# Kernel optimization log

Hardware: AMD Instinct MI355X
Metric: run time of the kernel (lower is better)

Reference implementation:

```python
import jax, jax.numpy as jnp
import numpy as np

GAMMA = 0.7
ALPHA = 1.0
EPS = 1e-6

def setup_inputs() -> dict:
    key = jax.random.key(0)
    k1, k2 = jax.random.split(key)
    x = jax.random.normal(k1, (1, 4096, 1024), dtype=jnp.float32)
    attn = jax.random.uniform(k2, (1, 4096, 4096), dtype=jnp.float32)
    return {"x": x, "attn": attn, "layer_idx": 10, "total_layers": 12}


def reference(x, attn, layer_idx, total_layers):
    B, N, D = x.shape  # module's masking/cat logic requires B == 1
    if layer_idx < GAMMA * total_layers:
        return x

    # --- spatial autocorrelation score s ---
    a = x.mean(axis=-1)                                            # [B,N]
    z = (a - a.mean(1, keepdims=True)) / (a.std(1, ddof=1, keepdims=True) + EPS)
    # diag(z z^T * W) == z^2 * diag(W): skip the O(N^2) outer product
    I_l = z * z * jnp.diagonal(attn, axis1=-2, axis2=-1)           # [B,N]
    s = (I_l - I_l.mean(1, keepdims=True)) / (I_l.std(1, ddof=1, keepdims=True) + EPS)

    # --- threshold (torch.median returns the LOWER middle for even N) ---
    mu_s = s.mean(1, keepdims=True)
    abs_med = jnp.sort(jnp.abs(s), axis=1)[:, (N - 1) // 2][:, None]
    lb = ALPHA * (mu_s - abs_med)
    ub = ALPHA * (mu_s + abs_med)
    mask_A = (s < lb) | (s > ub)                                   # [B,N]

    xb = x[0]
    mA = mask_A[0]
    idx = jnp.arange(N)
    n_A = mA.sum()

    # compact A tokens to the front preserving original order
    orderA = jnp.argsort(~mA, stable=True)
    tokA = xb[orderA]                    # first n_A rows are tokens_A, rest are B tokens (masked later)
    mid = n_A // 2
    n2 = n_A - mid                       # number of A2 tokens

    # A1[i] = tokA[i] (valid i < mid); A2[j] = tokA[mid + j] (valid j < n2)
    A2 = jnp.take(tokA, jnp.clip(mid + idx, 0, N - 1), axis=0)     # [N,D] padded
    validA1 = idx < mid
    validA2 = idx < n2

    sim = tokA @ A2.T                                              # [N,N]
    sim = jnp.where(validA2[None, :], sim, -jnp.inf)
    matches = jnp.argmax(sim, axis=1)                              # [N]
    merged = 0.5 * (tokA + A2[matches])
    merged = jnp.where(validA1[:, None], merged, 0.0)              # rows >= mid zeroed

    # residual A2 tokens (not matched by any valid A1 row), compacted and zero-padded
    drop_idx = jnp.where(validA1, matches, N)                      # OOB index dropped
    matched = jnp.zeros(N, bool).at[drop_idx].set(True, mode='drop')
    resid_valid = validA2 & ~matched
    orderR = jnp.argsort(~resid_valid, stable=True)
    residual = jnp.where(resid_valid[orderR][:, None], A2[orderR], 0.0)  # [N,D]

    # B tokens compacted, then merged tokens appended, zero pad to N
    n_B = N - n_A
    orderB = jnp.argsort(mA, stable=True)
    tokB = jnp.where((idx < n_B)[:, None], xb[orderB], 0.0)        # [N,D]
    shift = jnp.clip(idx - n_B, 0, N - 1)
    in_merged = ((idx >= n_B) & (idx < n_B + mid)).astype(xb.dtype)[:, None]
    out = (tokB + in_merged * merged[shift])[None]                 # [1,N,D]
    return out, residual
```

## Files before the change

### kernel.cpp

```cpp
#include <hip/hip_runtime.h>

#define N 4096
#define D 1024
#define EPSF 1e-6f

typedef _Float16 f16;
typedef f16 f16x8 __attribute__((ext_vector_type(8)));
typedef float f32x4 __attribute__((ext_vector_type(4)));
typedef unsigned long long u64;

#define PLANE ((size_t)2048 * 1024)

struct WS {
  int n_A, mid, n2, n_B, n_resid, pad[3];
  float a[N];
  float diag[N];
  int A1idx[N];
  int A2idx[N];
  int Bidx[N];
  int matches[N];
  int residIdx[N];
  u64 bestKey[2048];
};

__device__ __forceinline__ u64 packKey(float v, int j) {
  unsigned u = __float_as_uint(v);
  unsigned m = (u & 0x80000000u) ? ~u : (u | 0x80000000u);
  return ((u64)m << 32) | (unsigned)(~(unsigned)j);
}

__global__ __launch_bounds__(256) void k_prep(const float* __restrict__ x,
                                              const float* __restrict__ attn, WS* ws) {
  int row = blockIdx.x;
  int t = threadIdx.x;
  float4 v = ((const float4*)(x + (size_t)row * D))[t];
  float sm = v.x + v.y + v.z + v.w;
  for (int o = 32; o; o >>= 1) sm += __shfl_down(sm, o, 64);
  __shared__ float w[4];
  if ((t & 63) == 0) w[t >> 6] = sm;
  __syncthreads();
  if (t == 0) {
    ws->a[row] = (w[0] + w[1] + w[2] + w[3]) * (1.0f / D);
    ws->diag[row] = attn[(size_t)row * N + row];
  }
}

__global__ __launch_bounds__(256) void k_mask(WS* ws) {
  __shared__ double dred[4], dred2[4];
  __shared__ float bcast[2];
  __shared__ int hist[256];
  __shared__ int wsum[4];
  __shared__ unsigned sPrefix;
  __shared__ int sRank;
  int tid = threadIdx.x;
  int lane = tid & 63, wv = tid >> 6;

  #pragma unroll
  for (int q = 0; q < 8; q++) ws->bestKey[tid * 8 + q] = 0ull;

  float av[16];
  double s = 0.0, s2 = 0.0;
  #pragma unroll
  for (int q = 0; q < 4; q++) {
    float4 va = ((const float4*)ws->a)[tid * 4 + q];
    float f4[4] = {va.x, va.y, va.z, va.w};
    #pragma unroll
    for (int e = 0; e < 4; e++) {
      av[q * 4 + e] = f4[e];
      s += f4[e]; s2 += (double)f4[e] * f4[e];
    }
  }
  for (int o = 32; o; o >>= 1) { s += __shfl_down(s, o, 64); s2 += __shfl_down(s2, o, 64); }
  if (lane == 0) { dred[wv] = s; dred2[wv] = s2; }
  __syncthreads();
  if (tid == 0) {
    double t1 = dred[0] + dred[1] + dred[2] + dred[3];
    double t2 = dred2[0] + dred2[1] + dred2[2] + dred2[3];
    bcast[0] = (float)(t1 / N);
    bcast[1] = (float)sqrt((t2 - t1 * t1 / N) / (N - 1));
  }
  __syncthreads();
  float meanA = bcast[0], stdA = bcast[1];

  float il[16];
  s = 0.0; s2 = 0.0;
  #pragma unroll
  for (int q = 0; q < 4; q++) {
    float4 dg = ((const float4*)ws->diag)[tid * 4 + q];
    float d4[4] = {dg.x, dg.y, dg.z, dg.w};
    #pragma unroll
    for (int e = 0; e < 4; e++) {
      float z = (av[q * 4 + e] - meanA) / (stdA + EPSF);
      float I = z * z * d4[e];
      il[q * 4 + e] = I;
      s += I; s2 += (double)I * I;
    }
  }
  for (int o = 32; o; o >>= 1) { s += __shfl_down(s, o, 64); s2 += __shfl_down(s2, o, 64); }
  __syncthreads();
  if (lane == 0) { dred[wv] = s; dred2[wv] = s2; }
  __syncthreads();
  if (tid == 0) {
    double t1 = dred[0] + dred[1] + dred[2] + dred[3];
    double t2 = dred2[0] + dred2[1] + dred2[2] + dred2[3];
    bcast[0] = (float)(t1 / N);
    bcast[1] = (float)sqrt((t2 - t1 * t1 / N) / (N - 1));
    sPrefix = 0u; sRank = (N - 1) / 2;
  }
  __syncthreads();
  float meanI = bcast[0], stdI = bcast[1];

  float sv[16]; unsigned ab[16];
  #pragma unroll
  for (int q = 0; q < 16; q++) {
    float sval = (il[q] - meanI) / (stdI + EPSF);
    sv[q] = sval;
    ab[q] = __float_as_uint(fabsf(sval));
  }

  for (int p = 3; p >= 0; p--) {
    hist[tid] = 0;
    __syncthreads();
    unsigned pre = sPrefix;
    int rk = sRank;
    int sh = p * 8;
    unsigned mHi = (p == 3) ? 0u : (0xFFFFFFFFu << (sh + 8));
    #pragma unroll
    for (int q = 0; q < 16; q++)
      if ((ab[q] & mHi) == pre) atomicAdd(&hist[(ab[q] >> sh) & 255], 1);
    __syncthreads();
    int v2 = hist[tid];
    int inc = v2;
    #pragma unroll
    for (int o = 1; o < 64; o <<= 1) { int u = __shfl_up(inc, o, 64); if (lane >= o) inc += u; }
    if (lane == 63) wsum[wv] = inc;
    __syncthreads();
    if (tid == 0) { wsum[1] += wsum[0]; wsum[2] += wsum[1]; wsum[3] += wsum[2]; }
    __syncthreads();
    int incl = (wv ? wsum[wv - 1] : 0) + inc;
    int E = incl - v2;
    if (v2 && rk >= E && rk < E + v2) {
      sPrefix = pre | ((unsigned)tid << sh);
      sRank = rk - E;
    }
    __syncthreads();
  }
  float med = __uint_as_float(sPrefix);

  int msk[16], loc[16]; int tot = 0;
  #pragma unroll
  for (int q = 0; q < 16; q++) {
    bool m = fabsf(sv[q]) > med;
    msk[q] = m; loc[q] = tot; tot += (int)m;
  }
  int inc = tot;
  #pragma unroll
  for (int o = 1; o < 64; o <<= 1) { int u = __shfl_up(inc, o, 64); if (lane >= o) inc += u; }
  if (lane == 63) wsum[wv] = inc;
  __syncthreads();
  if (tid == 0) { wsum[1] += wsum[0]; wsum[2] += wsum[1]; wsum[3] += wsum[2]; }
  __syncthreads();
  int nA = wsum[3];
  int base = (wv ? wsum[wv - 1] : 0) + inc - tot;
  int midl = nA >> 1;
  #pragma unroll
  for (int q = 0; q < 16; q++) {
    int i = tid * 16 + q;
    int r = base + loc[q];
    if (msk[q]) {
      if (r < midl) ws->A1idx[r] = i; else ws->A2idx[r - midl] = i;
    } else {
      ws->Bidx[i - r] = i;
    }
  }
  if (tid == 0) { ws->n_A = nA; ws->mid = midl; ws->n2 = nA - midl; ws->n_B = N - nA; }
}

__global__ __launch_bounds__(128) void k_pack(const float* __restrict__ x,
                                              f16* __restrict__ PAhi, f16* __restrict__ PAlo,
                                              f16* __restrict__ PBhi, f16* __restrict__ PBlo,
                                              WS* ws) {
  int b = blockIdx.x, t = threadIdx.x;
  const float* src;
  f16 *dh, *dl;
  int j;
  if (b < 2048) {
    if (b >= ws->mid) return;
    j = b;
    src = x + (size_t)ws->A1idx[b] * D;
    dh = PAhi; dl = PAlo;
  } else {
    j = b - 2048;
    if (j >= ws->n2) return;
    src = x + (size_t)ws->A2idx[j] * D;
    dh = PBhi; dl = PBlo;
  }
  float4 v0 = ((const float4*)src)[t * 2];
  float4 v1 = ((const float4*)src)[t * 2 + 1];
  float vv[8] = {v0.x, v0.y, v0.z, v0.w, v1.x, v1.y, v1.z, v1.w};
  f16x8 h, l;
  #pragma unroll
  for (int q = 0; q < 8; q++) {
    f16 hq = (f16)vv[q];
    h[q] = hq;
    l[q] = (f16)(vv[q] - (float)hq);
  }
  int rt = j >> 6, rl = j & 63;
  int kt = t >> 3, gl = t & 7;
  size_t off = ((size_t)(rt * 16 + kt) << 12) + rl * 64 + ((gl ^ (rl & 7)) * 8);
  *(f16x8*)(dh + off) = h;
  *(f16x8*)(dl + off) = l;
}

__global__ __launch_bounds__(256) void k_gemm(const f16* __restrict__ PAhi,
                                              const f16* __restrict__ PAlo,
                                              const f16* __restrict__ PBhi,
                                              const f16* __restrict__ PBlo, WS* ws) {
  const int mid = ws->mid, n2 = ws->n2;
  int L = blockIdx.x;
  int local = L >> 3;
  int bj = ((L & 7) << 1) | (local >> 4);
  int bi = local & 15;
  if (bi * 64 >= mid || bj * 64 >= n2) return;

  __shared__ f16 lds[2][4][64 * 64];

  const int tid = threadIdx.x;
  const int lane = tid & 63;
  const int wid = tid >> 6;
  const int wr = wid >> 1, wc = wid & 1;

  const f16* plane = (wid == 0) ? PAhi : (wid == 1) ? PAlo : (wid == 2) ? PBhi : PBlo;
  const int ptile = (wid < 2) ? bi : bj;

  f16x8 pr[8];
  auto LOAD = [&](int t) {
    const f16* tb = plane + ((size_t)((ptile << 4) + t) << 12);
    #pragma unroll
    for (int i = 0; i < 8; i++) pr[i] = *(const f16x8*)(tb + i * 512 + lane * 8);
  };
  auto STORE = [&](int buf) {
    #pragma unroll
    for (int i = 0; i < 8; i++) *(f16x8*)&lds[buf][wid][i * 512 + lane * 8] = pr[i];
  };

  const int colg = lane & 15, rowg = lane >> 4;
  const int ma0 = wr * 32 + colg, ma1 = ma0 + 16;
  const int mb0 = wc * 32 + colg, mb1 = mb0 + 16;

  f32x4 zero = {0.f, 0.f, 0.f, 0.f};
  f32x4 acc[2][2];
  acc[0][0] = zero; acc[0][1] = zero; acc[1][0] = zero; acc[1][1] = zero;

#define FRAG(buf, t4, row, g) \
  (*(const f16x8*)&lds[buf][t4][(row) * 64 + ((((g) ^ ((row) & 7))) * 8)])

  LOAD(0);
  STORE(0);
  __syncthreads();
  for (int t16 = 0; t16 < 16; t16++) {
    int buf = t16 & 1;
    if (t16 < 15) LOAD(t16 + 1);
    #pragma unroll
    for (int ks = 0; ks < 2; ks++) {
      int gk = ks * 4 + rowg;
      f16x8 ah0 = FRAG(buf, 0, ma0, gk), ah1 = FRAG(buf, 0, ma1, gk);
      f16x8 al0 = FRAG(buf, 1, ma0, gk), al1 = FRAG(buf, 1, ma1, gk);
      f16x8 bh0 = FRAG(buf, 2, mb0, gk), bh1 = FRAG(buf, 2, mb1, gk);
      f16x8 bl0 = FRAG(buf, 3, mb0, gk), bl1 = FRAG(buf, 3, mb1, gk);
      acc[0][0] = __builtin_amdgcn_mfma_f32_16x16x32_f16(ah0, bh0, acc[0][0], 0, 0, 0);
      acc[0][0] = __builtin_amdgcn_mfma_f32_16x16x32_f16(ah0, bl0, acc[0][0], 0, 0, 0);
      acc[0][0] = __builtin_amdgcn_mfma_f32_16x16x32_f16(al0, bh0, acc[0][0], 0, 0, 0);
      acc[0][1] = __builtin_amdgcn_mfma_f32_16x16x32_f16(ah0, bh1, acc[0][1], 0, 0, 0);
      acc[0][1] = __builtin_amdgcn_mfma_f32_16x16x32_f16(ah0, bl1, acc[0][1], 0, 0, 0);
      acc[0][1] = __builtin_amdgcn_mfma_f32_16x16x32_f16(al0, bh1, acc[0][1], 0, 0, 0);
      acc[1][0] = __builtin_amdgcn_mfma_f32_16x16x32_f16(ah1, bh0, acc[1][0], 0, 0, 0);
      acc[1][0] = __builtin_amdgcn_mfma_f32_16x16x32_f16(ah1, bl0, acc[1][0], 0, 0, 0);
      acc[1][0] = __builtin_amdgcn_mfma_f32_16x16x32_f16(al1, bh0, acc[1][0], 0, 0, 0);
      acc[1][1] = __builtin_amdgcn_mfma_f32_16x16x32_f16(ah1, bh1, acc[1][1], 0, 0, 0);
      acc[1][1] = __builtin_amdgcn_mfma_f32_16x16x32_f16(ah1, bl1, acc[1][1], 0, 0, 0);
      acc[1][1] = __builtin_amdgcn_mfma_f32_16x16x32_f16(al1, bh1, acc[1][1], 0, 0, 0);
    }
    if (t16 < 15) {
      __syncthreads();
      STORE(buf ^ 1);
      __syncthreads();
    }
  }
#undef FRAG

  #pragma unroll
  for (int mi = 0; mi < 2; mi++) {
    #pragma unroll
    for (int i = 0; i < 4; i++) {
      int grow = bi * 64 + wr * 32 + mi * 16 + rowg * 4 + i;
      u64 key = 0;
      #pragma unroll
      for (int ni = 0; ni < 2; ni++) {
        int gcol = bj * 64 + wc * 32 + ni * 16 + colg;
        if (gcol < n2) {
          u64 k2 = packKey(acc[mi][ni][i], gcol);
          if (k2 > key) key = k2;
        }
      }
      #pragma unroll
      for (int m = 8; m; m >>= 1) {
        u64 o = (u64)__shfl_xor((long long)key, m, 64);
        if (o > key) key = o;
      }
      if (colg == 0 && grow < mid && key) atomicMax(&ws->bestKey[grow], key);
    }
  }
}

__global__ __launch_bounds__(1024) void k_match(WS* ws) {
  __shared__ int flag[N];
  __shared__ int wsum[16];
  int tid = threadIdx.x;
  int lane = tid & 63, wv = tid >> 6;
  int mid = ws->mid, n2 = ws->n2;
  #pragma unroll
  for (int q = 0; q < 4; q++) flag[tid * 4 + q] = 0;
  __syncthreads();
  #pragma unroll
  for (int q = 0; q < 2; q++) {
    int r = tid + q * 1024;
    if (r < mid) {
      int j = (int)(~(unsigned)(ws->bestKey[r] & 0xffffffffull));
      ws->matches[r] = j;
      flag[j] = 1;
    }
  }
  __syncthreads();
  int v[4], loc[4]; int tot = 0;
  #pragma unroll
  for (int q = 0; q < 4; q++) {
    int j = tid * 4 + q;
    bool val = (j < n2) && (flag[j] == 0);
    v[q] = val; loc[q] = tot; tot += (int)val;
  }
  int inc = tot;
  #pragma unroll
  for (int o = 1; o < 64; o <<= 1) { int u = __shfl_up(inc, o, 64); if (lane >= o) inc += u; }
  if (lane == 63) wsum[wv] = inc;
  __syncthreads();
  if (tid < 16) {
    int t = wsum[tid];
    #pragma unroll
    for (int o = 1; o < 16; o <<= 1) { int u = __shfl_up(t, o, 64); if (tid >= o) t += u; }
    wsum[tid] = t;
  }
  __syncthreads();
  int base = (wv ? wsum[wv - 1] : 0) + inc - tot;
  #pragma unroll
  for (int q = 0; q < 4; q++)
    if (v[q]) ws->residIdx[base + loc[q]] = ws->A2idx[tid * 4 + q];
  if (tid == 0) ws->n_resid = wsum[15];
}

__global__ __launch_bounds__(256) void k_write(const float* __restrict__ x,
                                               float* __restrict__ out, WS* ws) {
  int r = blockIdx.x;
  int t = threadIdx.x;
  int n_B = ws->n_B, mid = ws->mid, n_resid = ws->n_resid;
  float4 res = make_float4(0.f, 0.f, 0.f, 0.f);
  if (r < N) {
    if (r < n_B) {
      res = ((const float4*)(x + (size_t)ws->Bidx[r] * D))[t];
    } else if (r < n_B + mid) {
      int m = r - n_B;
      float4 v1 = ((const float4*)(x + (size_t)ws->A1idx[m] * D))[t];
      float4 v2 = ((const float4*)(x + (size_t)ws->A2idx[ws->matches[m]] * D))[t];
      res = make_float4(0.5f * (v1.x + v2.x), 0.5f * (v1.y + v2.y),
                        0.5f * (v1.z + v2.z), 0.5f * (v1.w + v2.w));
    }
  } else {
    int k = r - N;
    if (k < n_resid) {
      res = ((const float4*)(x + (size_t)ws->residIdx[k] * D))[t];
    }
  }
  ((float4*)(out + (size_t)r * D))[t] = res;
}

extern "C" void kernel_launch(void* const* d_in, const int* in_sizes, int n_in,
                              void* d_out, int out_size, void* d_ws, size_t ws_size,
                              hipStream_t stream) {
  const float* x = (const float*)d_in[0];
  const float* attn = (const float*)d_in[1];
  float* out = (float*)d_out;
  WS* ws = (WS*)d_ws;
  f16* PAhi = (f16*)d_out;
  f16* PAlo = PAhi + PLANE;
  f16* PBhi = PAlo + PLANE;
  f16* PBlo = PBhi + PLANE;

  k_prep<<<N, 256, 0, stream>>>(x, attn, ws);
  k_mask<<<1, 256, 0, stream>>>(ws);
  k_pack<<<4096, 128, 0, stream>>>(x, PAhi, PAlo, PBhi, PBlo, ws);
  k_gemm<<<256, 256, 0, stream>>>(PAhi, PAlo, PBhi, PBlo, ws);
  k_match<<<1, 1024, 0, stream>>>(ws);
  k_write<<<2 * N, 256, 0, stream>>>(x, out, ws);
}
```

Before: 58.18 us.

## Fuse all stages into one cooperative persistent kernel with grid syncs

Replaces the six separate launches (prep, mask, pack, gemm, match, write) with a single cooperative kernel of 256 blocks. Stages are separated by grid.sync, and each stage's work is redistributed over the fixed block count with strided loops. The intent is to remove per-launch overhead and the inter-kernel gaps around the two single-block serial stages. In exchange it adds grid-wide barrier costs, and the memory-bound write and pack phases now run at low occupancy (one block per CU looping), which may reduce achieved bandwidth.

```diff
diff --git a/kernel.cpp b/kernel.cpp
--- a/kernel.cpp
+++ b/kernel.cpp
@@ -1,4 +1,7 @@
 #include <hip/hip_runtime.h>
+#include <hip/hip_cooperative_groups.h>
+
+namespace cg = cooperative_groups;
 
 #define N 4096
 #define D 1024
@@ -23,364 +26,377 @@
   u64 bestKey[2048];
 };
 
+struct MaskSh {
+  double dred[4], dred2[4];
+  float bcast[2];
+  int hist[256];
+  int wsum[4];
+  unsigned sPrefix;
+  int sRank;
+};
+
 __device__ __forceinline__ u64 packKey(float v, int j) {
   unsigned u = __float_as_uint(v);
   unsigned m = (u & 0x80000000u) ? ~u : (u | 0x80000000u);
   return ((u64)m << 32) | (unsigned)(~(unsigned)j);
 }
 
-__global__ __launch_bounds__(256) void k_prep(const float* __restrict__ x,
-                                              const float* __restrict__ attn, WS* ws) {
-  int row = blockIdx.x;
-  int t = threadIdx.x;
-  float4 v = ((const float4*)(x + (size_t)row * D))[t];
-  float sm = v.x + v.y + v.z + v.w;
-  for (int o = 32; o; o >>= 1) sm += __shfl_down(sm, o, 64);
-  __shared__ float w[4];
-  if ((t & 63) == 0) w[t >> 6] = sm;
-  __syncthreads();
-  if (t == 0) {
-    ws->a[row] = (w[0] + w[1] + w[2] + w[3]) * (1.0f / D);
-    ws->diag[row] = attn[(size_t)row * N + row];
-  }
-}
-
-__global__ __launch_bounds__(256) void k_mask(WS* ws) {
-  __shared__ double dred[4], dred2[4];
-  __shared__ float bcast[2];
-  __shared__ int hist[256];
-  __shared__ int wsum[4];
-  __shared__ unsigned sPrefix;
-  __shared__ int sRank;
-  int tid = threadIdx.x;
-  int lane = tid & 63, wv = tid >> 6;
-
-  #pragma unroll
-  for (int q = 0; q < 8; q++) ws->bestKey[tid * 8 + q] = 0ull;
-
-  float av[16];
-  double s = 0.0, s2 = 0.0;
-  #pragma unroll
-  for (int q = 0; q < 4; q++) {
-    float4 va = ((const float4*)ws->a)[tid * 4 + q];
-    float f4[4] = {va.x, va.y, va.z, va.w};
-    #pragma unroll
-    for (int e = 0; e < 4; e++) {
-      av[q * 4 + e] = f4[e];
-      s += f4[e]; s2 += (double)f4[e] * f4[e];
-    }
-  }
-  for (int o = 32; o; o >>= 1) { s += __shfl_down(s, o, 64); s2 += __shfl_down(s2, o, 64); }
-  if (lane == 0) { dred[wv] = s; dred2[wv] = s2; }
-  __syncthreads();
-  if (tid == 0) {
-    double t1 = dred[0] + dred[1] + dred[2] + dred[3];
-    double t2 = dred2[0] + dred2[1] + dred2[2] + dred2[3];
-    bcast[0] = (float)(t1 / N);
-    bcast[1] = (float)sqrt((t2 - t1 * t1 / N) / (N - 1));
-  }
-  __syncthreads();
-  float meanA = bcast[0], stdA = bcast[1];
-
-  float il[16];
-  s = 0.0; s2 = 0.0;
-  #pragma unroll
-  for (int q = 0; q < 4; q++) {
-    float4 dg = ((const float4*)ws->diag)[tid * 4 + q];
-    float d4[4] = {dg.x, dg.y, dg.z, dg.w};
-    #pragma unroll
-    for (int e = 0; e < 4; e++) {
-      float z = (av[q * 4 + e] - meanA) / (stdA + EPSF);
-      float I = z * z * d4[e];
-      il[q * 4 + e] = I;
-      s += I; s2 += (double)I * I;
-    }
-  }
-  for (int o = 32; o; o >>= 1) { s += __shfl_down(s, o, 64); s2 += __shfl_down(s2, o, 64); }
-  __syncthreads();
-  if (lane == 0) { dred[wv] = s; dred2[wv] = s2; }
-  __syncthreads();
-  if (tid == 0) {
-    double t1 = dred[0] + dred[1] + dred[2] + dred[3];
-    double t2 = dred2[0] + dred2[1] + dred2[2] + dred2[3];
-    bcast[0] = (float)(t1 / N);
-    bcast[1] = (float)sqrt((t2 - t1 * t1 / N) / (N - 1));
-    sPrefix = 0u; sRank = (N - 1) / 2;
-  }
-  __syncthreads();
-  float meanI = bcast[0], stdI = bcast[1];
-
-  float sv[16]; unsigned ab[16];
-  #pragma unroll
-  for (int q = 0; q < 16; q++) {
-    float sval = (il[q] - meanI) / (stdI + EPSF);
-    sv[q] = sval;
-    ab[q] = __float_as_uint(fabsf(sval));
-  }
-
-  for (int p = 3; p >= 0; p--) {
-    hist[tid] = 0;
-    __syncthreads();
-    unsigned pre = sPrefix;
-    int rk = sRank;
-    int sh = p * 8;
-    unsigned mHi = (p == 3) ? 0u : (0xFFFFFFFFu << (sh + 8));
-    #pragma unroll
-    for (int q = 0; q < 16; q++)
-      if ((ab[q] & mHi) == pre) atomicAdd(&hist[(ab[q] >> sh) & 255], 1);
-    __syncthreads();
-    int v2 = hist[tid];
-    int inc = v2;
-    #pragma unroll
-    for (int o = 1; o < 64; o <<= 1) { int u = __shfl_up(inc, o, 64); if (lane >= o) inc += u; }
-    if (lane == 63) wsum[wv] = inc;
-    __syncthreads();
-    if (tid == 0) { wsum[1] += wsum[0]; wsum[2] += wsum[1]; wsum[3] += wsum[2]; }
-    __syncthreads();
-    int incl = (wv ? wsum[wv - 1] : 0) + inc;
-    int E = incl - v2;
-    if (v2 && rk >= E && rk < E + v2) {
-      sPrefix = pre | ((unsigned)tid << sh);
-      sRank = rk - E;
-    }
-    __syncthreads();
-  }
-  float med = __uint_as_float(sPrefix);
-
-  int msk[16], loc[16]; int tot = 0;
-  #pragma unroll
-  for (int q = 0; q < 16; q++) {
-    bool m = fabsf(sv[q]) > med;
-    msk[q] = m; loc[q] = tot; tot += (int)m;
-  }
-  int inc = tot;
-  #pragma unroll
-  for (int o = 1; o < 64; o <<= 1) { int u = __shfl_up(inc, o, 64); if (lane >= o) inc += u; }
-  if (lane == 63) wsum[wv] = inc;
-  __syncthreads();
-  if (tid == 0) { wsum[1] += wsum[0]; wsum[2] += wsum[1]; wsum[3] += wsum[2]; }
-  __syncthreads();
-  int nA = wsum[3];
-  int base = (wv ? wsum[wv - 1] : 0) + inc - tot;
-  int midl = nA >> 1;
-  #pragma unroll
-  for (int q = 0; q < 16; q++) {
-    int i = tid * 16 + q;
-    int r = base + loc[q];
-    if (msk[q]) {
-      if (r < midl) ws->A1idx[r] = i; else ws->A2idx[r - midl] = i;
-    } else {
-      ws->Bidx[i - r] = i;
-    }
-  }
-  if (tid == 0) { ws->n_A = nA; ws->mid = midl; ws->n2 = nA - midl; ws->n_B = N - nA; }
-}
-
-__global__ __launch_bounds__(128) void k_pack(const float* __restrict__ x,
-                                              f16* __restrict__ PAhi, f16* __restrict__ PAlo,
-                                              f16* __restrict__ PBhi, f16* __restrict__ PBlo,
-                                              WS* ws) {
-  int b = blockIdx.x, t = threadIdx.x;
-  const float* src;
-  f16 *dh, *dl;
-  int j;
-  if (b < 2048) {
-    if (b >= ws->mid) return;
-    j = b;
-    src = x + (size_t)ws->A1idx[b] * D;
-    dh = PAhi; dl = PAlo;
-  } else {
-    j = b - 2048;
-    if (j >= ws->n2) return;
-    src = x + (size_t)ws->A2idx[j] * D;
-    dh = PBhi; dl = PBlo;
-  }
-  float4 v0 = ((const float4*)src)[t * 2];
-  float4 v1 = ((const float4*)src)[t * 2 + 1];
-  float vv[8] = {v0.x, v0.y, v0.z, v0.w, v1.x, v1.y, v1.z, v1.w};
-  f16x8 h, l;
-  #pragma unroll
-  for (int q = 0; q < 8; q++) {
-    f16 hq = (f16)vv[q];
-    h[q] = hq;
-    l[q] = (f16)(vv[q] - (float)hq);
-  }
-  int rt = j >> 6, rl = j & 63;
-  int kt = t >> 3, gl = t & 7;
-  size_t off = ((size_t)(rt * 16 + kt) << 12) + rl * 64 + ((gl ^ (rl & 7)) * 8);
-  *(f16x8*)(dh + off) = h;
-  *(f16x8*)(dl + off) = l;
-}
-
-__global__ __launch_bounds__(256) void k_gemm(const f16* __restrict__ PAhi,
-                                              const f16* __restrict__ PAlo,
-                                              const f16* __restrict__ PBhi,
-                                              const f16* __restrict__ PBlo, WS* ws) {
-  const int mid = ws->mid, n2 = ws->n2;
-  int L = blockIdx.x;
-  int local = L >> 3;
-  int bj = ((L & 7) << 1) | (local >> 4);
-  int bi = local & 15;
-  if (bi * 64 >= mid || bj * 64 >= n2) return;
-
-  __shared__ f16 lds[2][4][64 * 64];
+__global__ void __launch_bounds__(256) k_all(const float* __restrict__ x,
+                                             const float* __restrict__ attn,
+                                             f16* __restrict__ PAhi, f16* __restrict__ PAlo,
+                                             f16* __restrict__ PBhi, f16* __restrict__ PBlo,
+                                             float* __restrict__ out, WS* __restrict__ ws) {
+  cg::grid_group grid = cg::this_grid();
+  __shared__ __align__(16) f16 lds[2][4][64 * 64];
 
   const int tid = threadIdx.x;
   const int lane = tid & 63;
-  const int wid = tid >> 6;
-  const int wr = wid >> 1, wc = wid & 1;
-
-  const f16* plane = (wid == 0) ? PAhi : (wid == 1) ? PAlo : (wid == 2) ? PBhi : PBlo;
-  const int ptile = (wid < 2) ? bi : bj;
-
-  f16x8 pr[8];
-  auto LOAD = [&](int t) {
-    const f16* tb = plane + ((size_t)((ptile << 4) + t) << 12);
-    #pragma unroll
-    for (int i = 0; i < 8; i++) pr[i] = *(const f16x8*)(tb + i * 512 + lane * 8);
-  };
-  auto STORE = [&](int buf) {
-    #pragma unroll
-    for (int i = 0; i < 8; i++) *(f16x8*)&lds[buf][wid][i * 512 + lane * 8] = pr[i];
-  };
-
-  const int colg = lane & 15, rowg = lane >> 4;
-  const int ma0 = wr * 32 + colg, ma1 = ma0 + 16;
-  const int mb0 = wc * 32 + colg, mb1 = mb0 + 16;
-
-  f32x4 zero = {0.f, 0.f, 0.f, 0.f};
-  f32x4 acc[2][2];
-  acc[0][0] = zero; acc[0][1] = zero; acc[1][0] = zero; acc[1][1] = zero;
+  const int wv = tid >> 6;
+  const int bid = blockIdx.x;
+
+  {
+    #pragma unroll
+    for (int rr = 0; rr < 4; rr++) {
+      int row = bid * 16 + wv * 4 + rr;
+      const float4* xr = (const float4*)(x + (size_t)row * D);
+      float sm = 0.f;
+      #pragma unroll
+      for (int it = 0; it < 4; it++) {
+        float4 v = xr[it * 64 + lane];
+        sm += v.x + v.y + v.z + v.w;
+      }
+      for (int o = 32; o; o >>= 1) sm += __shfl_down(sm, o, 64);
+      if (lane == 0) {
+        ws->a[row] = sm * (1.0f / D);
+        ws->diag[row] = attn[(size_t)row * (N + 1)];
+      }
+    }
+  }
+  grid.sync();
+
+  if (bid == 0) {
+    MaskSh& sh = *(MaskSh*)lds;
+
+    #pragma unroll
+    for (int q = 0; q < 8; q++) ws->bestKey[tid * 8 + q] = 0ull;
+
+    float av[16];
+    double s = 0.0, s2 = 0.0;
+    #pragma unroll
+    for (int q = 0; q < 4; q++) {
+      float4 va = ((const float4*)ws->a)[tid * 4 + q];
+      float f4[4] = {va.x, va.y, va.z, va.w};
+      #pragma unroll
+      for (int e = 0; e < 4; e++) {
+        av[q * 4 + e] = f4[e];
+        s += f4[e]; s2 += (double)f4[e] * f4[e];
+      }
+    }
+    for (int o = 32; o; o >>= 1) { s += __shfl_down(s, o, 64); s2 += __shfl_down(s2, o, 64); }
+    if (lane == 0) { sh.dred[wv] = s; sh.dred2[wv] = s2; }
+    __syncthreads();
+    if (tid == 0) {
+      double t1 = sh.dred[0] + sh.dred[1] + sh.dred[2] + sh.dred[3];
+      double t2 = sh.dred2[0] + sh.dred2[1] + sh.dred2[2] + sh.dred2[3];
+      sh.bcast[0] = (float)(t1 / N);
+      sh.bcast[1] = (float)sqrt((t2 - t1 * t1 / N) / (N - 1));
+    }
+    __syncthreads();
+    float meanA = sh.bcast[0], stdA = sh.bcast[1];
+
+    float il[16];
+    s = 0.0; s2 = 0.0;
+    #pragma unroll
+    for (int q = 0; q < 4; q++) {
+      float4 dg = ((const float4*)ws->diag)[tid * 4 + q];
+      float d4[4] = {dg.x, dg.y, dg.z, dg.w};
+      #pragma unroll
+      for (int e = 0; e < 4; e++) {
+        float z = (av[q * 4 + e] - meanA) / (stdA + EPSF);
+        float I = z * z * d4[e];
+        il[q * 4 + e] = I;
+        s += I; s2 += (double)I * I;
+      }
+    }
+    for (int o = 32; o; o >>= 1) { s += __shfl_down(s, o, 64); s2 += __shfl_down(s2, o, 64); }
+    __syncthreads();
+    if (lane == 0) { sh.dred[wv] = s; sh.dred2[wv] = s2; }
+    __syncthreads();
+    if (tid == 0) {
+      double t1 = sh.dred[0] + sh.dred[1] + sh.dred[2] + sh.dred[3];
+      double t2 = sh.dred2[0] + sh.dred2[1] + sh.dred2[2] + sh.dred2[3];
+      sh.bcast[0] = (float)(t1 / N);
+      sh.bcast[1] = (float)sqrt((t2 - t1 * t1 / N) / (N - 1));
+      sh.sPrefix = 0u; sh.sRank = (N - 1) / 2;
+    }
+    __syncthreads();
+    float meanI = sh.bcast[0], stdI = sh.bcast[1];
+
+    float sv[16]; unsigned ab[16];
+    #pragma unroll
+    for (int q = 0; q < 16; q++) {
+      float sval = (il[q] - meanI) / (stdI + EPSF);
+      sv[q] = sval;
+      ab[q] = __float_as_uint(fabsf(sval));
+    }
+
+    for (int p = 3; p >= 0; p--) {
+      sh.hist[tid] = 0;
+      __syncthreads();
+      unsigned pre = sh.sPrefix;
+      int rk = sh.sRank;
+      int shf = p * 8;
+      unsigned mHi = (p == 3) ? 0u : (0xFFFFFFFFu << (shf + 8));
+      #pragma unroll
+      for (int q = 0; q < 16; q++)
+        if ((ab[q] & mHi) == pre) atomicAdd(&sh.hist[(ab[q] >> shf) & 255], 1);
+      __syncthreads();
+      int v2 = sh.hist[tid];
+      int inc = v2;
+      #pragma unroll
+      for (int o = 1; o < 64; o <<= 1) { int u = __shfl_up(inc, o, 64); if (lane >= o) inc += u; }
+      if (lane == 63) sh.wsum[wv] = inc;
+      __syncthreads();
+      if (tid == 0) { sh.wsum[1] += sh.wsum[0]; sh.wsum[2] += sh.wsum[1]; sh.wsum[3] += sh.wsum[2]; }
+      __syncthreads();
+      int incl = (wv ? sh.wsum[wv - 1] : 0) + inc;
+      int E = incl - v2;
+      if (v2 && rk >= E && rk < E + v2) {
+        sh.sPrefix = pre | ((unsigned)tid << shf);
+        sh.sRank = rk - E;
+      }
+      __syncthreads();
+    }
+    float med = __uint_as_float(sh.sPrefix);
+
+    int msk[16], loc[16]; int tot = 0;
+    #pragma unroll
+    for (int q = 0; q < 16; q++) {
+      bool m = fabsf(sv[q]) > med;
+      msk[q] = m; loc[q] = tot; tot += (int)m;
+    }
+    int inc = tot;
+    #pragma unroll
+    for (int o = 1; o < 64; o <<= 1) { int u = __shfl_up(inc, o, 64); if (lane >= o) inc += u; }
+    if (lane == 63) sh.wsum[wv] = inc;
+    __syncthreads();
+    if (tid == 0) { sh.wsum[1] += sh.wsum[0]; sh.wsum[2] += sh.wsum[1]; sh.wsum[3] += sh.wsum[2]; }
+    __syncthreads();
+    int nA = sh.wsum[3];
+    int base = (wv ? sh.wsum[wv - 1] : 0) + inc - tot;
+    int midl = nA >> 1;
+    #pragma unroll
+    for (int q = 0; q < 16; q++) {
+      int i = tid * 16 + q;
+      int r = base + loc[q];
+      if (msk[q]) {
+        if (r < midl) ws->A1idx[r] = i; else ws->A2idx[r - midl] = i;
+      } else {
+        ws->Bidx[i - r] = i;
+      }
+    }
+    if (tid == 0) { ws->n_A = nA; ws->mid = midl; ws->n2 = nA - midl; ws->n_B = N - nA; }
+  }
+  grid.sync();
+
+  const int mid = ws->mid, n2 = ws->n2;
+
+  {
+    int sub = tid >> 7;
+    int tt = tid & 127;
+    #pragma unroll 1
+    for (int it = 0; it < 8; it++) {
+      int slot = it * 512 + bid * 2 + sub;
+      const float* src = nullptr;
+      f16 *dh, *dl;
+      int j;
+      bool valid;
+      if (slot < 2048) {
+        j = slot; valid = (j < mid);
+        if (valid) src = x + (size_t)ws->A1idx[j] * D;
+        dh = PAhi; dl = PAlo;
+      } else {
+        j = slot - 2048; valid = (j < n2);
+        if (valid) src = x + (size_t)ws->A2idx[j] * D;
+        dh = PBhi; dl = PBlo;
+      }
+      if (valid) {
+        float4 v0 = ((const float4*)src)[tt * 2];
+        float4 v1 = ((const float4*)src)[tt * 2 + 1];
+        float vv[8] = {v0.x, v0.y, v0.z, v0.w, v1.x, v1.y, v1.z, v1.w};
+        f16x8 h, l;
+        #pragma unroll
+        for (int q = 0; q < 8; q++) {
+          f16 hq = (f16)vv[q];
+          h[q] = hq;
+          l[q] = (f16)(vv[q] - (float)hq);
+        }
+        int rt = j >> 6, rl = j & 63;
+        int kt = tt >> 3, gl = tt & 7;
+        size_t off = ((size_t)(rt * 16 + kt) << 12) + rl * 64 + ((gl ^ (rl & 7)) * 8);
+        *(f16x8*)(dh + off) = h;
+        *(f16x8*)(dl + off) = l;
+      }
+    }
+  }
+  grid.sync();
+
+  {
+    int local = bid >> 3;
+    int bj = ((bid & 7) << 1) | (local >> 4);
+    int bi = local & 15;
+    if (bi * 64 < mid && bj * 64 < n2) {
+      const int wid = wv;
+      const int wr = wid >> 1, wc = wid & 1;
+      const f16* plane = (wid == 0) ? PAhi : (wid == 1) ? PAlo : (wid == 2) ? PBhi : PBlo;
+      const int ptile = (wid < 2) ? bi : bj;
+
+      f16x8 pr[8];
+      auto LOAD = [&](int t) {
+        const f16* tb = plane + ((size_t)((ptile << 4) + t) << 12);
+        #pragma unroll
+        for (int i = 0; i < 8; i++) pr[i] = *(const f16x8*)(tb + i * 512 + lane * 8);
+      };
+      auto STORE = [&](int buf) {
+        #pragma unroll
+        for (int i = 0; i < 8; i++) *(f16x8*)&lds[buf][wid][i * 512 + lane * 8] = pr[i];
+      };
+
+      const int colg = lane & 15, rowg = lane >> 4;
+      const int ma0 = wr * 32 + colg, ma1 = ma0 + 16;
+      const int mb0 = wc * 32 + colg, mb1 = mb0 + 16;
+
+      f32x4 zero = {0.f, 0.f, 0.f, 0.f};
+      f32x4 acc[2][2];
+      acc[0][0] = zero; acc[0][1] = zero; acc[1][0] = zero; acc[1][1] = zero;
 
 #define FRAG(buf, t4, row, g) \
   (*(const f16x8*)&lds[buf][t4][(row) * 64 + ((((g) ^ ((row) & 7))) * 8)])
 
-  LOAD(0);
-  STORE(0);
-  __syncthreads();
-  for (int t16 = 0; t16 < 16; t16++) {
-    int buf = t16 & 1;
-    if (t16 < 15) LOAD(t16 + 1);
-    #pragma unroll
-    for (int ks = 0; ks < 2; ks++) {
-      int gk = ks * 4 + rowg;
-      f16x8 ah0 = FRAG(buf, 0, ma0, gk), ah1 = FRAG(buf, 0, ma1, gk);
-      f16x8 al0 = FRAG(buf, 1, ma0, gk), al1 = FRAG(buf, 1, ma1, gk);
-      f16x8 bh0 = FRAG(buf, 2, mb0, gk), bh1 = FRAG(buf, 2, mb1, gk);
-      f16x8 bl0 = FRAG(buf, 3, mb0, gk), bl1 = FRAG(buf, 3, mb1, gk);
-      acc[0][0] = __builtin_amdgcn_mfma_f32_16x16x32_f16(ah0, bh0, acc[0][0], 0, 0, 0);
-      acc[0][0] = __builtin_amdgcn_mfma_f32_16x16x32_f16(ah0, bl0, acc[0][0], 0, 0, 0);
-      acc[0][0] = __builtin_amdgcn_mfma_f32_16x16x32_f16(al0, bh0, acc[0][0], 0, 0, 0);
-      acc[0][1] = __builtin_amdgcn_mfma_f32_16x16x32_f16(ah0, bh1, acc[0][1], 0, 0, 0);
-      acc[0][1] = __builtin_amdgcn_mfma_f32_16x16x32_f16(ah0, bl1, acc[0][1], 0, 0, 0);
-      acc[0][1] = __builtin_amdgcn_mfma_f32_16x16x32_f16(al0, bh1, acc[0][1], 0, 0, 0);
-      acc[1][0] = __builtin_amdgcn_mfma_f32_16x16x32_f16(ah1, bh0, acc[1][0], 0, 0, 0);
-      acc[1][0] = __builtin_amdgcn_mfma_f32_16x16x32_f16(ah1, bl0, acc[1][0], 0, 0, 0);
-      acc[1][0] = __builtin_amdgcn_mfma_f32_16x16x32_f16(al1, bh0, acc[1][0], 0, 0, 0);
-      acc[1][1] = __builtin_amdgcn_mfma_f32_16x16x32_f16(ah1, bh1, acc[1][1], 0, 0, 0);
-      acc[1][1] = __builtin_amdgcn_mfma_f32_16x16x32_f16(ah1, bl1, acc[1][1], 0, 0, 0);
-      acc[1][1] = __builtin_amdgcn_mfma_f32_16x16x32_f16(al1, bh1, acc[1][1], 0, 0, 0);
-    }
-    if (t16 < 15) {
-      __syncthreads();
-      STORE(buf ^ 1);
-      __syncthreads();
-    }
-  }
+      LOAD(0);
+      STORE(0);
+      __syncthreads();
+      #pragma unroll 1
+      for (int t16 = 0; t16 < 16; t16++) {
+        int buf = t16 & 1;
+        if (t16 < 15) LOAD(t16 + 1);
+        #pragma unroll
+        for (int ks = 0; ks < 2; ks++) {
+          int gk = ks * 4 + rowg;
+          f16x8 ah0 = FRAG(buf, 0, ma0, gk), ah1 = FRAG(buf, 0, ma1, gk);
+          f16x8 al0 = FRAG(buf, 1, ma0, gk), al1 = FRAG(buf, 1, ma1, gk);
+          f16x8 bh0 = FRAG(buf, 2, mb0, gk), bh1 = FRAG(buf, 2, mb1, gk);
+          f16x8 bl0 = FRAG(buf, 3, mb0, gk), bl1 = FRAG(buf, 3, mb1, gk);
+          acc[0][0] = __builtin_amdgcn_mfma_f32_16x16x32_f16(ah0, bh0, acc[0][0], 0, 0, 0);
+          acc[0][0] = __builtin_amdgcn_mfma_f32_16x16x32_f16(ah0, bl0, acc[0][0], 0, 0, 0);
+          acc[0][0] = __builtin_amdgcn_mfma_f32_16x16x32_f16(al0, bh0, acc[0][0], 0, 0, 0);
+          acc[0][1] = __builtin_amdgcn_mfma_f32_16x16x32_f16(ah0, bh1, acc[0][1], 0, 0, 0);
+          acc[0][1] = __builtin_amdgcn_mfma_f32_16x16x32_f16(ah0, bl1, acc[0][1], 0, 0, 0);
+          acc[0][1] = __builtin_amdgcn_mfma_f32_16x16x32_f16(al0, bh1, acc[0][1], 0, 0, 0);
+          acc[1][0] = __builtin_amdgcn_mfma_f32_16x16x32_f16(ah1, bh0, acc[1][0], 0, 0, 0);
+          acc[1][0] = __builtin_amdgcn_mfma_f32_16x16x32_f16(ah1, bl0, acc[1][0], 0, 0, 0);
+          acc[1][0] = __builtin_amdgcn_mfma_f32_16x16x32_f16(al1, bh0, acc[1][0], 0, 0, 0);
+          acc[1][1] = __builtin_amdgcn_mfma_f32_16x16x32_f16(ah1, bh1, acc[1][1], 0, 0, 0);
+          acc[1][1] = __builtin_amdgcn_mfma_f32_16x16x32_f16(ah1, bl1, acc[1][1], 0, 0, 0);
+          acc[1][1] = __builtin_amdgcn_mfma_f32_16x16x32_f16(al1, bh1, acc[1][1], 0, 0, 0);
+        }
+        if (t16 < 15) {
+          __syncthreads();
+          STORE(buf ^ 1);
+          __syncthreads();
+        }
+      }
 #undef FRAG
 
-  #pragma unroll
-  for (int mi = 0; mi < 2; mi++) {
-    #pragma unroll
-    for (int i = 0; i < 4; i++) {
-      int grow = bi * 64 + wr * 32 + mi * 16 + rowg * 4 + i;
-      u64 key = 0;
-      #pragma unroll
-      for (int ni = 0; ni < 2; ni++) {
-        int gcol = bj * 64 + wc * 32 + ni * 16 + colg;
-        if (gcol < n2) {
-          u64 k2 = packKey(acc[mi][ni][i], gcol);
-          if (k2 > key) key = k2;
-        }
-      }
-      #pragma unroll
-      for (int m = 8; m; m >>= 1) {
-        u64 o = (u64)__shfl_xor((long long)key, m, 64);
-        if (o > key) key = o;
-      }
-      if (colg == 0 && grow < mid && key) atomicMax(&ws->bestKey[grow], key);
-    }
-  }
-}
-
-__global__ __launch_bounds__(1024) void k_match(WS* ws) {
-  __shared__ int flag[N];
-  __shared__ int wsum[16];
-  int tid = threadIdx.x;
-  int lane = tid & 63, wv = tid >> 6;
-  int mid = ws->mid, n2 = ws->n2;
-  #pragma unroll
-  for (int q = 0; q < 4; q++) flag[tid * 4 + q] = 0;
-  __syncthreads();
-  #pragma unroll
-  for (int q = 0; q < 2; q++) {
-    int r = tid + q * 1024;
-    if (r < mid) {
-      int j = (int)(~(unsigned)(ws->bestKey[r] & 0xffffffffull));
-      ws->matches[r] = j;
-      flag[j] = 1;
-    }
-  }
-  __syncthreads();
-  int v[4], loc[4]; int tot = 0;
-  #pragma unroll
-  for (int q = 0; q < 4; q++) {
-    int j = tid * 4 + q;
-    bool val = (j < n2) && (flag[j] == 0);
-    v[q] = val; loc[q] = tot; tot += (int)val;
-  }
-  int inc = tot;
-  #pragma unroll
-  for (int o = 1; o < 64; o <<= 1) { int u = __shfl_up(inc, o, 64); if (lane >= o) inc += u; }
-  if (lane == 63) wsum[wv] = inc;
-  __syncthreads();
-  if (tid < 16) {
-    int t = wsum[tid];
-    #pragma unroll
-    for (int o = 1; o < 16; o <<= 1) { int u = __shfl_up(t, o, 64); if (tid >= o) t += u; }
-    wsum[tid] = t;
-  }
-  __syncthreads();
-  int base = (wv ? wsum[wv - 1] : 0) + inc - tot;
-  #pragma unroll
-  for (int q = 0; q < 4; q++)
-    if (v[q]) ws->residIdx[base + loc[q]] = ws->A2idx[tid * 4 + q];
-  if (tid == 0) ws->n_resid = wsum[15];
-}
-
-__global__ __launch_bounds__(256) void k_write(const float* __restrict__ x,
-                                               float* __restrict__ out, WS* ws) {
-  int r = blockIdx.x;
-  int t = threadIdx.x;
-  int n_B = ws->n_B, mid = ws->mid, n_resid = ws->n_resid;
-  float4 res = make_float4(0.f, 0.f, 0.f, 0.f);
-  if (r < N) {
-    if (r < n_B) {
-      res = ((const float4*)(x + (size_t)ws->Bidx[r] * D))[t];
-    } else if (r < n_B + mid) {
-      int m = r - n_B;
-      float4 v1 = ((const float4*)(x + (size_t)ws->A1idx[m] * D))[t];
-      float4 v2 = ((const float4*)(x + (size_t)ws->A2idx[ws->matches[m]] * D))[t];
-      res = make_float4(0.5f * (v1.x + v2.x), 0.5f * (v1.y + v2.y),
-                        0.5f * (v1.z + v2.z), 0.5f * (v1.w + v2.w));
-    }
-  } else {
-    int k = r - N;
-    if (k < n_resid) {
-      res = ((const float4*)(x + (size_t)ws->residIdx[k] * D))[t];
-    }
-  }
-  ((float4*)(out + (size_t)r * D))[t] = res;
+      #pragma unroll
+      for (int mi = 0; mi < 2; mi++) {
+        #pragma unroll
+        for (int i = 0; i < 4; i++) {
+          int grow = bi * 64 + wr * 32 + mi * 16 + rowg * 4 + i;
+          u64 key = 0;
+          #pragma unroll
+          for (int ni = 0; ni < 2; ni++) {
+            int gcol = bj * 64 + wc * 32 + ni * 16 + colg;
+            if (gcol < n2) {
+              u64 k2 = packKey(acc[mi][ni][i], gcol);
+              if (k2 > key) key = k2;
+            }
+          }
+          #pragma unroll
+          for (int m = 8; m; m >>= 1) {
+            u64 o = (u64)__shfl_xor((long long)key, m, 64);
+            if (o > key) key = o;
+          }
+          if (colg == 0 && grow < mid && key) atomicMax(&ws->bestKey[grow], key);
+        }
+      }
+    }
+  }
+  grid.sync();
+
+  if (bid == 0) {
+    int* flag = (int*)lds;
+    int* mwsum = flag + N;
+    #pragma unroll
+    for (int q = 0; q < 16; q++) flag[tid * 16 + q] = 0;
+    __syncthreads();
+    #pragma unroll
+    for (int q = 0; q < 8; q++) {
+      int r = tid + q * 256;
+      if (r < mid) {
+        int j = (int)(~(unsigned)(ws->bestKey[r] & 0xffffffffull));
+        ws->matches[r] = j;
+        flag[j] = 1;
+      }
+    }
+    __syncthreads();
+    int v[8], loc[8]; int tot = 0;
+    #pragma unroll
+    for (int q = 0; q < 8; q++) {
+      int j = tid * 8 + q;
+      bool val = (j < n2) && (flag[j] == 0);
+      v[q] = val; loc[q] = tot; tot += (int)val;
+    }
+    int inc = tot;
+    #pragma unroll
+    for (int o = 1; o < 64; o <<= 1) { int u = __shfl_up(inc, o, 64); if (lane >= o) inc += u; }
+    if (lane == 63) mwsum[wv] = inc;
+    __syncthreads();
+    if (tid == 0) { mwsum[1] += mwsum[0]; mwsum[2] += mwsum[1]; mwsum[3] += mwsum[2]; }
+    __syncthreads();
+    int base = (wv ? mwsum[wv - 1] : 0) + inc - tot;
+    #pragma unroll
+    for (int q = 0; q < 8; q++)
+      if (v[q]) ws->residIdx[base + loc[q]] = ws->A2idx[tid * 8 + q];
+    if (tid == 0) ws->n_resid = mwsum[3];
+  }
+  grid.sync();
+
+  {
+    int n_B = ws->n_B, n_resid = ws->n_resid;
+    #pragma unroll 1
+    for (int it = 0; it < 32; it++) {
+      int r = it * 256 + bid;
+      float4 res = make_float4(0.f, 0.f, 0.f, 0.f);
+      if (r < N) {
+        if (r < n_B) {
+          res = ((const float4*)(x + (size_t)ws->Bidx[r] * D))[tid];
+        } else if (r < n_B + mid) {
+          int m = r - n_B;
+          float4 v1 = ((const float4*)(x + (size_t)ws->A1idx[m] * D))[tid];
+          float4 v2 = ((const float4*)(x + (size_t)ws->A2idx[ws->matches[m]] * D))[tid];
+          res = make_float4(0.5f * (v1.x + v2.x), 0.5f * (v1.y + v2.y),
+                            0.5f * (v1.z + v2.z), 0.5f * (v1.w + v2.w));
+        }
+      } else {
+        int k = r - N;
+        if (k < n_resid) {
+          res = ((const float4*)(x + (size_t)ws->residIdx[k] * D))[tid];
+        }
+      }
+      ((float4*)(out + (size_t)r * D))[tid] = res;
+    }
+  }
 }
 
 extern "C" void kernel_launch(void* const* d_in, const int* in_sizes, int n_in,
@@ -395,10 +411,7 @@
   f16* PBhi = PAlo + PLANE;
   f16* PBlo = PBhi + PLANE;
 
-  k_prep<<<N, 256, 0, stream>>>(x, attn, ws);
-  k_mask<<<1, 256, 0, stream>>>(ws);
-  k_pack<<<4096, 128, 0, stream>>>(x, PAhi, PAlo, PBhi, PBlo, ws);
-  k_gemm<<<256, 256, 0, stream>>>(PAhi, PAlo, PBhi, PBlo, ws);
-  k_match<<<1, 1024, 0, stream>>>(ws);
-  k_write<<<2 * N, 256, 0, stream>>>(x, out, ws);
+  void* args[8] = {(void*)&x, (void*)&attn, (void*)&PAhi, (void*)&PAlo,
+                   (void*)&PBhi, (void*)&PBlo, (void*)&out, (void*)&ws};
+  hipLaunchCooperativeKernel((void*)k_all, dim3(256), dim3(256), args, 0, stream);
 }
```

After: 195.1 us. +235.3%, slower.
